# Kernel optimization log

Measured on AMD Instinct MI355X. Metric: run time of the kernel, lower is better.

The kernel has to match this reference:

```python
import jax, jax.numpy as jnp
import numpy as np

N_USERS = 30000
N_ITEMS = 20000
EMBED = 64
N_UI_LAYERS = 2
MASK_RATE = 0.1
MODEL_CAT = 0.02
USER_CAT = 0.3
ITEM_CAT = 0.3
NNZ = 600000


def setup_inputs() -> dict:
    key = jax.random.key(0)
    ks = jax.random.split(key, 16)
    ui_rows = jax.random.randint(ks[0], (NNZ,), 0, N_USERS, dtype=jnp.int64 if jax.config.jax_enable_x64 else jnp.int32)
    ui_cols = jax.random.randint(ks[1], (NNZ,), 0, N_ITEMS, dtype=ui_rows.dtype)
    ui_vals = jax.random.uniform(ks[2], (NNZ,), dtype=jnp.float32) * 0.1
    image_feats = jax.random.normal(ks[3], (N_ITEMS, 4096), dtype=jnp.float32)
    text_feats = jax.random.normal(ks[4], (N_ITEMS, 768), dtype=jnp.float32)
    user_feats0 = jax.random.normal(ks[5], (N_USERS, 1536), dtype=jnp.float32)
    item_title = jax.random.normal(ks[6], (N_ITEMS, 1536), dtype=jnp.float32)
    W_img = jax.random.normal(ks[7], (EMBED, 4096), dtype=jnp.float32) * 0.02
    b_img = jnp.zeros((EMBED,), jnp.float32)
    W_txt = jax.random.normal(ks[8], (EMBED, 768), dtype=jnp.float32) * 0.02
    b_txt = jnp.zeros((EMBED,), jnp.float32)
    W_usr = jax.random.normal(ks[9], (EMBED, 1536), dtype=jnp.float32) * 0.02
    b_usr = jnp.zeros((EMBED,), jnp.float32)
    W_itm = jax.random.normal(ks[10], (EMBED, 1536), dtype=jnp.float32) * 0.02
    b_itm = jnp.zeros((EMBED,), jnp.float32)
    user_id_emb = jax.random.normal(ks[11], (N_USERS, EMBED), dtype=jnp.float32) * 0.02
    item_id_emb = jax.random.normal(ks[12], (N_ITEMS, EMBED), dtype=jnp.float32) * 0.02
    return dict(ui_rows=ui_rows, ui_cols=ui_cols, ui_vals=ui_vals,
                image_feats=image_feats, text_feats=text_feats,
                user_feats0=user_feats0, item_title=item_title,
                W_img=W_img, b_img=b_img, W_txt=W_txt, b_txt=b_txt,
                W_usr=W_usr, b_usr=b_usr, W_itm=W_itm, b_itm=b_itm,
                user_id_emb=user_id_emb, item_id_emb=item_id_emb)


def _l2n(x):
    # F.normalize(x, p=2, dim=1)
    n = jnp.sqrt(jnp.sum(x * x, axis=1, keepdims=True))
    return x / jnp.maximum(n, 1e-12)


def reference(ui_rows, ui_cols, ui_vals, image_feats, text_feats, user_feats0, item_title,
              W_img, b_img, W_txt, b_txt, W_usr, b_usr, W_itm, b_itm,
              user_id_emb, item_id_emb):
    # sparse.mm(ui_graph, x): gather item rows, scale by edge vals, scatter-add to users
    def spmm_ui(x):
        return jax.ops.segment_sum(ui_vals[:, None] * x[ui_cols], ui_rows, num_segments=N_USERS)

    def spmm_iu(x):  # transpose graph
        return jax.ops.segment_sum(ui_vals[:, None] * x[ui_rows], ui_cols, num_segments=N_ITEMS)

    # --- feature masking (randperm with fixed key) ---
    num_mask = int(MASK_RATE * N_ITEMS)
    perm = jax.random.permutation(jax.random.key(42), N_ITEMS)
    mask_nodes = perm[:num_mask]
    img_m = image_feats.at[mask_nodes].set(image_feats.mean(0))
    txt_m = text_feats.at[mask_nodes].set(text_feats.mean(0))
    itm_m = item_title.at[mask_nodes].set(item_title.mean(0))

    # --- dense projections (dropout p=0 -> identity) ---
    raw_image = image_feats @ W_img.T + b_img
    raw_text = text_feats @ W_txt.T + b_txt
    raw_item = item_title @ W_itm.T + b_itm
    img_e = img_m @ W_img.T + b_img
    txt_e = txt_m @ W_txt.T + b_txt
    usr_e = user_feats0 @ W_usr.T + b_usr
    itm_e = itm_m @ W_itm.T + b_itm

    # --- modality graph propagation (args.layers=1; torch loop recomputes from fixed feats) ---
    image_user = spmm_ui(img_e)
    image_item = spmm_iu(image_user)
    text_user = spmm_ui(txt_e)
    text_item = spmm_iu(text_user)

    user_feat_from_item = spmm_ui(itm_e)
    item_feats_out = spmm_iu(user_feat_from_item)
    item_prof = spmm_iu(usr_e)
    user_prof = spmm_ui(item_prof)

    # --- id-embedding LightGCN-ish propagation ---
    u = user_id_emb
    i = item_id_emb
    u_list = [u]
    i_list = [i]
    for l in range(N_UI_LAYERS):
        if l == N_UI_LAYERS - 1:
            u = jax.nn.softmax(spmm_ui(i), axis=-1)
            i = jax.nn.softmax(spmm_iu(u), axis=-1)
        else:
            u = spmm_ui(i)
            i = spmm_iu(u)
        u_list.append(u)
        i_list.append(i)
    u_g = jnp.mean(jnp.stack(u_list), axis=0)
    i_g = jnp.mean(jnp.stack(i_list), axis=0)

    u_g = u_g + MODEL_CAT * _l2n(image_user) + MODEL_CAT * _l2n(text_user)
    i_g = i_g + MODEL_CAT * _l2n(image_item) + MODEL_CAT * _l2n(text_item)
    u_g = u_g + USER_CAT * _l2n(user_prof)
    i_g = i_g + USER_CAT * _l2n(item_prof)
    u_g = u_g + ITEM_CAT * _l2n(user_feat_from_item)
    i_g = i_g + ITEM_CAT * _l2n(item_feats_out)

    return (u_g, i_g, image_item, text_item, image_user, text_user, usr_e, item_feats_out,
            user_prof, item_prof, user_feat_from_item, mask_nodes,
            raw_image, raw_text, raw_item)
```

## Files before the change

kernel.cpp:

```cpp
#include <hip/hip_runtime.h>
#include <hip/hip_bf16.h>
#include <cstdint>
#include <cstddef>

#define NU 30000
#define NI 20000
#define NMASK 2000
#define NBUCK 2048

static inline int cdiv(int a, int b){ return (a + b - 1) / b; }

typedef __attribute__((ext_vector_type(8))) short bf16x8;
typedef __attribute__((ext_vector_type(4))) float f32x4;

__device__ __forceinline__ uint32_t rotl32(uint32_t x, int r){ return (x<<r)|(x>>(32-r)); }

__device__ __forceinline__ void tf2x32(uint32_t k0, uint32_t k1,
                                       uint32_t x0, uint32_t x1,
                                       uint32_t& o0, uint32_t& o1)
{
  uint32_t k2 = k0 ^ k1 ^ 0x1BD11BDAu;
  x0 += k0; x1 += k1;
#define TFR(r) { x0 += x1; x1 = rotl32(x1,(r)); x1 ^= x0; }
  TFR(13) TFR(15) TFR(26) TFR(6)
  x0 += k1; x1 += k2 + 1u;
  TFR(17) TFR(29) TFR(16) TFR(24)
  x0 += k2; x1 += k0 + 2u;
  TFR(13) TFR(15) TFR(26) TFR(6)
  x0 += k0; x1 += k1 + 3u;
  TFR(17) TFR(29) TFR(16) TFR(24)
  x0 += k1; x1 += k2 + 4u;
  TFR(13) TFR(15) TFR(26) TFR(6)
  x0 += k2; x1 += k0 + 5u;
#undef TFR
  o0 = x0; o1 = x1;
}

__device__ __forceinline__ ushort f2bf(float f){
  __hip_bfloat16 h = __float2bfloat16(f);
  return *reinterpret_cast<ushort*>(&h);
}
__device__ __forceinline__ uint32_t pk2(float a, float b){
  __hip_bfloat162 h = __float22bfloat162_rn(make_float2(a, b));
  return *reinterpret_cast<uint32_t*>(&h);
}
__device__ __forceinline__ uint2 f4_to_bf4(float4 v){
  __hip_bfloat162 h0 = __float22bfloat162_rn(make_float2(v.x, v.y));
  __hip_bfloat162 h1 = __float22bfloat162_rn(make_float2(v.z, v.w));
  return make_uint2(*reinterpret_cast<uint32_t*>(&h0), *reinterpret_cast<uint32_t*>(&h1));
}
__device__ __forceinline__ float lobf(uint32_t p){
  union { uint32_t u; float f; } c; c.u = p << 16; return c.f;
}
__device__ __forceinline__ float hibf(uint32_t p){
  union { uint32_t u; float f; } c; c.u = p & 0xffff0000u; return c.f;
}
__device__ __forceinline__ float bf2f(ushort h){
  union { uint32_t u; float f; } c; c.u = (uint32_t)h << 16; return c.f;
}

#define WTOTAL (64*(4096+768+1536+1536))
__global__ __launch_bounds__(256) void prep_kernel(
    uint32_t* __restrict__ bits1, uint32_t* __restrict__ bits2,
    int* __restrict__ h1, int* __restrict__ h2,
    const float* __restrict__ wi, const float* __restrict__ wt,
    const float* __restrict__ wm, const float* __restrict__ wu,
    ushort* __restrict__ wbf,
    const int* __restrict__ rows, const int* __restrict__ cols,
    int* __restrict__ cnt_u, int* __restrict__ cnt_i, int nnz)
{
  int i = blockIdx.x*256 + threadIdx.x;
  if (i < NI) {
    uint32_t c0,c1, s0,s1, t0,t1;
    tf2x32(0u,42u, 0u,0u, c0,c1);
    tf2x32(0u,42u, 0u,1u, s0,s1);
    tf2x32(c0,c1, 0u,1u, t0,t1);
    uint32_t o0,o1;
    tf2x32(s0,s1, 0u,(uint32_t)i, o0,o1);
    uint32_t b1 = o0^o1;
    tf2x32(t0,t1, 0u,(uint32_t)i, o0,o1);
    uint32_t b2 = o0^o1;
    bits1[i] = b1; bits2[i] = b2;
    atomicAdd(&h1[b1 >> 21], 1);
    atomicAdd(&h2[b2 >> 21], 1);
  }
  const int n0 = 64*4096, n1 = 64*768, n2 = 64*1536;
  for (int k = i; k < WTOTAL; k += gridDim.x*256) {
    float v;
    if (k < n0) v = wi[k];
    else if (k < n0+n1) v = wt[k-n0];
    else if (k < n0+n1+n2) v = wm[k-n0-n1];
    else v = wu[k-n0-n1-n2];
    wbf[k] = f2bf(v);
  }
  for (int k = i; k < nnz; k += gridDim.x*256) {
    atomicAdd(&cnt_u[rows[k]], 1);
    atomicAdd(&cnt_i[cols[k]], 1);
  }
}

__global__ __launch_bounds__(64) void exscan2_kernel(
    const int* __restrict__ h1, int* __restrict__ bb1,
    const int* __restrict__ h2, int* __restrict__ bb2)
{
  const int* cnt = blockIdx.x ? h2 : h1;
  int* ptr = blockIdx.x ? bb2 : bb1;
  int lane = threadIdx.x;
  int carry = 0;
  for (int base = 0; base < NBUCK; base += 64) {
    int i = base + lane;
    int v = cnt[i];
    int s = v;
#pragma unroll
    for (int off = 1; off < 64; off <<= 1) {
      int t = __shfl_up(s, off);
      if (lane >= off) s += t;
    }
    ptr[i] = carry + s - v;
    carry += __shfl(s, 63);
  }
  if (lane == 0) ptr[NBUCK] = carry;
}

__global__ __launch_bounds__(256) void scatter12_kernel(
    const uint32_t* __restrict__ bits1, const int* __restrict__ bb1, int* __restrict__ c1,
    uint64_t* __restrict__ barr1,
    const uint32_t* __restrict__ bits2, const int* __restrict__ bb2, int* __restrict__ c2,
    uint64_t* __restrict__ barr2, int n)
{
  int i = blockIdx.x*256 + threadIdx.x;
  if (i >= n) return;
  uint32_t k1 = bits1[i];
  int b = k1 >> 21;
  int p = bb1[b] + atomicAdd(&c1[b], 1);
  barr1[p] = ((uint64_t)k1 << 32) | (uint32_t)i;
  uint32_t k2 = bits2[i];
  b = k2 >> 21;
  p = bb2[b] + atomicAdd(&c2[b], 1);
  barr2[p] = ((uint64_t)k2 << 32) | (uint32_t)i;
}

template<int FINAL>
__global__ __launch_bounds__(256) void rank_bucket_kernel(
    const uint64_t* __restrict__ barr, const int* __restrict__ bptr,
    uint32_t* __restrict__ perm, float* __restrict__ mask_out, int* __restrict__ flag,
    int n)
{
  int p = blockIdx.x*256 + threadIdx.x;
  if (p >= n) return;
  uint64_t mk = barr[p];
  int b = (int)(mk >> 53);
  int p0 = bptr[b], p1 = bptr[b+1];
  int r = p0;
  for (int q = p0; q < p1; ++q) r += (int)(barr[q] < mk);
  uint32_t i = (uint32_t)mk;
  if (!FINAL) {
    perm[r] = i;
  } else if (r < NMASK) {
    uint32_t v = perm[i];
    mask_out[r] = (float)v;
    flag[v] = 1;
  }
}

#define RB_I 313
#define RB_U 469
__global__ __launch_bounds__(256) void gemm_all_kernel(
    const float* __restrict__ Xi, const float* __restrict__ Xt,
    const float* __restrict__ Xm, const float* __restrict__ Xu,
    const ushort* __restrict__ wbf,
    ushort* __restrict__ pb_img, ushort* __restrict__ pb_txt,
    ushort* __restrict__ pb_itm, ushort* __restrict__ pb_usr)
{
  __shared__ ushort Xs[64][72];
  __shared__ ushort Ws[64][72];
  const int bid = blockIdx.x;
  const float* X; const ushort* Wbf; ushort* pb;
  int N, K, klen, rb, ch;
  if (bid < RB_I*8) {
    X = Xi; Wbf = wbf; pb = pb_img; N = NI; K = 4096; klen = 512;
    rb = bid % RB_I; ch = bid / RB_I;
  } else if (bid < RB_I*12) {
    int l = bid - RB_I*8;
    X = Xt; Wbf = wbf + 64*4096; pb = pb_txt; N = NI; K = 768; klen = 192;
    rb = l % RB_I; ch = l / RB_I;
  } else if (bid < RB_I*16) {
    int l = bid - RB_I*12;
    X = Xm; Wbf = wbf + 64*(4096+768); pb = pb_itm; N = NI; K = 1536; klen = 384;
    rb = l % RB_I; ch = l / RB_I;
  } else {
    int l = bid - RB_I*16;
    X = Xu; Wbf = wbf + 64*(4096+768+1536); pb = pb_usr; N = NU; K = 1536; klen = 256;
    rb = l % RB_U; ch = l / RB_U;
  }
  const int tid = threadIdx.x;
  const int row0 = rb * 64;
  const int kbeg = ch * klen;
  const int lane = tid & 63;
  const int wr = tid >> 6;
  const int lrow = lane & 15;
  const int kslot = lane >> 4;
  f32x4 acc[4] = {f32x4{0,0,0,0},f32x4{0,0,0,0},f32x4{0,0,0,0},f32x4{0,0,0,0}};

  const int sr = tid >> 4;
  const int sc = (tid & 15) * 4;
  const int wrow = tid >> 2;
  const int wcol = (tid & 3) * 16;

  for (int k0 = kbeg; k0 < kbeg + klen; k0 += 64) {
#pragma unroll
    for (int i = 0; i < 4; ++i) {
      int r = sr + 16*i;
      int gr = row0 + r;
      float4 v = make_float4(0.f,0.f,0.f,0.f);
      if (gr < N) v = *reinterpret_cast<const float4*>(X + (size_t)gr*K + k0 + sc);
      *reinterpret_cast<uint2*>(&Xs[r][sc]) = f4_to_bf4(v);
    }
    {
      const ushort* wsrc = Wbf + (size_t)wrow*K + k0 + wcol;
      *reinterpret_cast<uint4*>(&Ws[wrow][wcol])   = *reinterpret_cast<const uint4*>(wsrc);
      *reinterpret_cast<uint4*>(&Ws[wrow][wcol+8]) = *reinterpret_cast<const uint4*>(wsrc + 8);
    }
    __syncthreads();
#pragma unroll
    for (int ks = 0; ks < 2; ++ks) {
      int kb = ks*32 + kslot*8;
      bf16x8 af = *reinterpret_cast<const bf16x8*>(&Xs[wr*16 + lrow][kb]);
#pragma unroll
      for (int ct = 0; ct < 4; ++ct) {
        bf16x8 bfr = *reinterpret_cast<const bf16x8*>(&Ws[ct*16 + lrow][kb]);
        acc[ct] = __builtin_amdgcn_mfma_f32_16x16x32_bf16(af, bfr, acc[ct], 0, 0, 0);
      }
    }
    __syncthreads();
  }
  ushort* pbc = pb + (size_t)ch * N * 64;
#pragma unroll
  for (int ct = 0; ct < 4; ++ct)
#pragma unroll
    for (int j = 0; j < 4; ++j) {
      int gr = row0 + wr*16 + kslot*4 + j;
      if (gr < N) pbc[(size_t)gr*64 + ct*16 + lrow] = f2bf(acc[ct][j]);
    }
}

__global__ __launch_bounds__(256) void reduce4_kernel(
    const ushort* __restrict__ pb_img, const ushort* __restrict__ pb_txt,
    const ushort* __restrict__ pb_itm, const ushort* __restrict__ pb_usr,
    const float* __restrict__ b_img, const float* __restrict__ b_txt,
    const float* __restrict__ b_itm, const float* __restrict__ b_usr,
    const float* __restrict__ idemb,
    float* __restrict__ o_ri, float* __restrict__ o_rt, float* __restrict__ o_rit,
    float* __restrict__ o_ue, ushort* __restrict__ ue_bf,
    uint2* __restrict__ pk_all, float* __restrict__ means)
{
  __shared__ float red[3][256];
  const int nI = NI*64, nUx = NU*64;
  int lane = threadIdx.x & 63;
  float sa = 0.f, sb = 0.f, sc = 0.f;
  for (int i = blockIdx.x*256 + threadIdx.x; i < nUx; i += gridDim.x*256) {
    int lc = i & 63;
    if (i < nI) {
      float s = b_img[lc];
#pragma unroll
      for (int c = 0; c < 8; ++c) s += bf2f(pb_img[(size_t)c*nI + i]);
      o_ri[i] = s;
      float t = b_txt[lc];
#pragma unroll
      for (int c = 0; c < 4; ++c) t += bf2f(pb_txt[(size_t)c*nI + i]);
      o_rt[i] = t;
      float u = b_itm[lc];
#pragma unroll
      for (int c = 0; c < 4; ++c) u += bf2f(pb_itm[(size_t)c*nI + i]);
      o_rit[i] = u;
      pk_all[i] = make_uint2(pk2(s, t), pk2(u, idemb[i]));
      sa += s; sb += t; sc += u;
    }
    float su = b_usr[lc];
#pragma unroll
    for (int c = 0; c < 6; ++c) su += bf2f(pb_usr[(size_t)c*nUx + i]);
    o_ue[i] = su; ue_bf[i] = f2bf(su);
  }
  red[0][threadIdx.x] = sa; red[1][threadIdx.x] = sb; red[2][threadIdx.x] = sc;
  __syncthreads();
  if (threadIdx.x < 64) {
#pragma unroll
    for (int q = 0; q < 3; ++q) {
      float t = red[q][lane]+red[q][64+lane]+red[q][128+lane]+red[q][192+lane];
      if (t != 0.f) atomicAdd(&means[q*64+lane], t * (1.f/NI));
    }
  }
}

__global__ __launch_bounds__(256) void scan_block2_kernel(
    const int* __restrict__ cnt_u, const int* __restrict__ cnt_i,
    int* __restrict__ part_u, int* __restrict__ part_i,
    int* __restrict__ bsum_u, int* __restrict__ bsum_i, int nbu)
{
  __shared__ int wsum[4];
  bool isU = (int)blockIdx.x < nbu;
  int blk = isU ? blockIdx.x : blockIdx.x - nbu;
  const int* cnt = isU ? cnt_u : cnt_i;
  int* part = isU ? part_u : part_i;
  int* bsum = isU ? bsum_u : bsum_i;
  int n = isU ? NU : NI;
  int i = blk*256 + threadIdx.x;
  int lane = threadIdx.x & 63;
  int w = threadIdx.x >> 6;
  int v = (i < n) ? cnt[i] : 0;
  int s = v;
#pragma unroll
  for (int off = 1; off < 64; off <<= 1) {
    int t = __shfl_up(s, off);
    if (lane >= off) s += t;
  }
  if (lane == 63) wsum[w] = s;
  __syncthreads();
  int wo = 0;
#pragma unroll
  for (int k = 0; k < 4; ++k) if (k < w) wo += wsum[k];
  if (i < n) part[i] = wo + s - v;
  if (threadIdx.x == 255) bsum[blk] = wo + s;
}

__global__ __launch_bounds__(64) void exscan2b_kernel(
    const int* __restrict__ bs_u, int* __restrict__ bp_u, int nbu,
    const int* __restrict__ bs_i, int* __restrict__ bp_i, int nbi)
{
  const int* cnt = blockIdx.x ? bs_i : bs_u;
  int* ptr = blockIdx.x ? bp_i : bp_u;
  int n = blockIdx.x ? nbi : nbu;
  int lane = threadIdx.x;
  int carry = 0;
  for (int base = 0; base < n; base += 64) {
    int i = base + lane;
    int v = (i < n) ? cnt[i] : 0;
    int s = v;
#pragma unroll
    for (int off = 1; off < 64; off <<= 1) {
      int t = __shfl_up(s, off);
      if (lane >= off) s += t;
    }
    if (i < n) ptr[i] = carry + s - v;
    carry += __shfl(s, 63);
  }
  if (lane == 0) ptr[n] = carry;
}

__global__ __launch_bounds__(256) void scan_add2_kernel(
    const int* __restrict__ part_u, const int* __restrict__ bp_u,
    const int* __restrict__ part_i, const int* __restrict__ bp_i,
    int* __restrict__ ptr_u, int* __restrict__ cur_u,
    int* __restrict__ ptr_i, int* __restrict__ cur_i, int nbu, int nbi)
{
  bool isU = (int)blockIdx.x < nbu;
  int blk = isU ? blockIdx.x : blockIdx.x - nbu;
  int n = isU ? NU : NI;
  const int* part = isU ? part_u : part_i;
  const int* bp = isU ? bp_u : bp_i;
  int* ptr = isU ? ptr_u : ptr_i;
  int* cur = isU ? cur_u : cur_i;
  int i = blk*256 + threadIdx.x;
  if (i < n) { int v = part[i] + bp[blk]; ptr[i] = v; cur[i] = v; }
  if (i == 0) ptr[n] = bp[isU ? nbu : nbi];
}

__global__ __launch_bounds__(256) void scatter_kernel(
    const int* __restrict__ rows, const int* __restrict__ cols, const float* __restrict__ vals,
    int* __restrict__ cur_u, int* __restrict__ cur_i,
    int* __restrict__ idx_u, float* __restrict__ val_u,
    int* __restrict__ idx_i, float* __restrict__ val_i, int nnz)
{
  int k = blockIdx.x*256 + threadIdx.x;
  if (k < nnz) {
    int r = rows[k], c = cols[k];
    float v = vals[k];
    int pu = atomicAdd(&cur_u[r], 1);
    idx_u[pu] = c; val_u[pu] = v;
    int pi = atomicAdd(&cur_i[c], 1);
    idx_i[pi] = r; val_i[pi] = v;
  }
}

__global__ __launch_bounds__(256) void spmm_user1_kernel(
    const int* __restrict__ ptr, const int* __restrict__ idx, const float* __restrict__ val,
    const uint2* __restrict__ pka,
    const int* __restrict__ flag, const float* __restrict__ means,
    float* __restrict__ iu, float* __restrict__ tu, float* __restrict__ ufi, float* __restrict__ u1,
    uint2* __restrict__ qa, int nrows)
{
  int row = blockIdx.x*4 + (threadIdx.x >> 6);
  int lane = threadIdx.x & 63;
  if (row >= nrows) return;
  int p0 = ptr[row], p1 = ptr[row+1];
  float m0 = means[lane], m1 = means[64+lane], m2 = means[128+lane];
  float a0=0.f, a1=0.f, a2=0.f, a3=0.f;
#define U1STEP(gg,ff,ww) { float x0,x1,x2, x3 = hibf(gg.y); \
    if (ff) { x0=m0; x1=m1; x2=m2; } \
    else { x0=lobf(gg.x); x1=hibf(gg.x); x2=lobf(gg.y); } \
    a0=fmaf(ww,x0,a0); a1=fmaf(ww,x1,a1); a2=fmaf(ww,x2,a2); a3=fmaf(ww,x3,a3); }
  int p = p0;
  for (; p + 8 <= p1; p += 8) {
    int j[8]; float w[8]; int f[8]; uint2 g[8];
#pragma unroll
    for (int q = 0; q < 8; ++q) { j[q]=idx[p+q]; w[q]=val[p+q]; }
#pragma unroll
    for (int q = 0; q < 8; ++q) { f[q]=flag[j[q]]; g[q]=pka[(size_t)j[q]*64+lane]; }
#pragma unroll
    for (int q = 0; q < 8; ++q) U1STEP(g[q],f[q],w[q])
  }
  for (; p + 4 <= p1; p += 4) {
    int j0=idx[p+0], j1=idx[p+1], j2=idx[p+2], j3=idx[p+3];
    float w0=val[p+0], w1=val[p+1], w2=val[p+2], w3=val[p+3];
    int f0=flag[j0], f1=flag[j1], f2=flag[j2], f3=flag[j3];
    uint2 g0=pka[(size_t)j0*64+lane], g1=pka[(size_t)j1*64+lane];
    uint2 g2=pka[(size_t)j2*64+lane], g3=pka[(size_t)j3*64+lane];
    U1STEP(g0,f0,w0) U1STEP(g1,f1,w1) U1STEP(g2,f2,w2) U1STEP(g3,f3,w3)
  }
  for (; p < p1; ++p) {
    int j = idx[p]; float v = val[p];
    uint2 g = pka[(size_t)j*64 + lane];
    int f = flag[j];
    U1STEP(g,f,v)
  }
#undef U1STEP
  size_t o = (size_t)row*64 + lane;
  iu[o]=a0; tu[o]=a1; ufi[o]=a2; u1[o]=a3;
  qa[o] = make_uint2(pk2(a0, a1), pk2(a2, a3));
}

__global__ __launch_bounds__(256) void spmm_item1_kernel(
    const int* __restrict__ ptr, const int* __restrict__ idx, const float* __restrict__ val,
    const uint2* __restrict__ qa, const ushort* __restrict__ ueh,
    float* __restrict__ ii, float* __restrict__ ti, float* __restrict__ ifo,
    float* __restrict__ i1, float* __restrict__ ip,
    uint32_t* __restrict__ qip1, int nrows)
{
  int row = blockIdx.x*4 + (threadIdx.x >> 6);
  int lane = threadIdx.x & 63;
  if (row >= nrows) return;
  int p0 = ptr[row], p1 = ptr[row+1];
  float a0=0.f, a1=0.f, a2=0.f, a3=0.f, a4=0.f;
#define I1STEP(gg,uu,ww) { \
    a0=fmaf(ww,lobf(gg.x),a0); a1=fmaf(ww,hibf(gg.x),a1); \
    a2=fmaf(ww,lobf(gg.y),a2); a3=fmaf(ww,hibf(gg.y),a3); \
    a4=fmaf(ww,bf2f(uu),a4); }
  int p = p0;
  for (; p + 8 <= p1; p += 8) {
    int j[8]; float w[8]; uint2 g[8]; ushort u[8];
#pragma unroll
    for (int q = 0; q < 8; ++q) { j[q]=idx[p+q]; w[q]=val[p+q]; }
#pragma unroll
    for (int q = 0; q < 8; ++q) {
      size_t b = (size_t)j[q]*64+lane;
      g[q]=qa[b]; u[q]=ueh[b];
    }
#pragma unroll
    for (int q = 0; q < 8; ++q) I1STEP(g[q],u[q],w[q])
  }
  for (; p + 4 <= p1; p += 4) {
    int j0=idx[p+0], j1=idx[p+1], j2=idx[p+2], j3=idx[p+3];
    float w0=val[p+0], w1=val[p+1], w2=val[p+2], w3=val[p+3];
    size_t b0=(size_t)j0*64+lane, b1=(size_t)j1*64+lane, b2=(size_t)j2*64+lane, b3=(size_t)j3*64+lane;
    uint2 g0=qa[b0], g1=qa[b1], g2=qa[b2], g3=qa[b3];
    ushort u0=ueh[b0], u1_=ueh[b1], u2_=ueh[b2], u3_=ueh[b3];
    I1STEP(g0,u0,w0) I1STEP(g1,u1_,w1) I1STEP(g2,u2_,w2) I1STEP(g3,u3_,w3)
  }
  for (; p < p1; ++p) {
    int j = idx[p]; float v = val[p];
    size_t b = (size_t)j*64 + lane;
    uint2 g = qa[b]; ushort u = ueh[b];
    I1STEP(g,u,v)
  }
#undef I1STEP
  size_t o = (size_t)row*64 + lane;
  ii[o]=a0; ti[o]=a1; ifo[o]=a2; i1[o]=a3; ip[o]=a4;
  qip1[o] = pk2(a4, a3);
}

__global__ __launch_bounds__(256) void user2_kernel(
    const int* __restrict__ ptr, const int* __restrict__ idx, const float* __restrict__ val,
    const uint32_t* __restrict__ qip1,
    const float* __restrict__ idemb, const float* __restrict__ u1,
    const float* __restrict__ iu, const float* __restrict__ tu, const float* __restrict__ ufi,
    float* __restrict__ up, ushort* __restrict__ u2h, float* __restrict__ ug, int nrows)
{
  int row = blockIdx.x*4 + (threadIdx.x >> 6);
  int lane = threadIdx.x & 63;
  if (row >= nrows) return;
  int p0 = ptr[row], p1 = ptr[row+1];
  float aup=0.f, au2=0.f;
  int p = p0;
  for (; p + 4 <= p1; p += 4) {
    int j0=idx[p+0], j1=idx[p+1], j2=idx[p+2], j3=idx[p+3];
    float w0=val[p+0], w1=val[p+1], w2=val[p+2], w3=val[p+3];
    uint32_t g0=qip1[(size_t)j0*64+lane], g1=qip1[(size_t)j1*64+lane];
    uint32_t g2=qip1[(size_t)j2*64+lane], g3=qip1[(size_t)j3*64+lane];
    aup=fmaf(w0,lobf(g0),aup); au2=fmaf(w0,hibf(g0),au2);
    aup=fmaf(w1,lobf(g1),aup); au2=fmaf(w1,hibf(g1),au2);
    aup=fmaf(w2,lobf(g2),aup); au2=fmaf(w2,hibf(g2),au2);
    aup=fmaf(w3,lobf(g3),aup); au2=fmaf(w3,hibf(g3),au2);
  }
  for (; p < p1; ++p) {
    int j = idx[p]; float v = val[p];
    uint32_t g = qip1[(size_t)j*64 + lane];
    aup = fmaf(v, lobf(g), aup);
    au2 = fmaf(v, hibf(g), au2);
  }
  float m = au2;
#pragma unroll
  for (int o2=32;o2;o2>>=1) m = fmaxf(m, __shfl_xor(m, o2));
  float e = expf(au2 - m);
  float s = e;
#pragma unroll
  for (int o2=32;o2;o2>>=1) s += __shfl_xor(s, o2);
  float u2 = e / s;
  size_t o = (size_t)row*64 + lane;
  up[o] = aup; u2h[o] = f2bf(u2);
  float e0 = idemb[o], e1 = u1[o];
  float v1 = iu[o], v2 = tu[o], v3 = aup, v4 = ufi[o];
  float n1=v1*v1, n2=v2*v2, n3=v3*v3, n4=v4*v4;
#pragma unroll
  for (int o2=32;o2;o2>>=1) {
    n1 += __shfl_xor(n1, o2); n2 += __shfl_xor(n2, o2);
    n3 += __shfl_xor(n3, o2); n4 += __shfl_xor(n4, o2);
  }
  n1 = fmaxf(sqrtf(n1), 1e-12f); n2 = fmaxf(sqrtf(n2), 1e-12f);
  n3 = fmaxf(sqrtf(n3), 1e-12f); n4 = fmaxf(sqrtf(n4), 1e-12f);
  ug[o] = (e0+e1+u2)*(1.f/3.f)
        + 0.02f*(v1/n1) + 0.02f*(v2/n2)
        + 0.30f*(v3/n3) + 0.30f*(v4/n4);
}

__global__ __launch_bounds__(256) void item2_kernel(
    const int* __restrict__ ptr, const int* __restrict__ idx, const float* __restrict__ val,
    const ushort* __restrict__ u2h,
    const float* __restrict__ idemb, const float* __restrict__ i1,
    const float* __restrict__ ii, const float* __restrict__ ti,
    const float* __restrict__ ip, const float* __restrict__ ifo,
    float* __restrict__ ig, int nrows)
{
  int row = blockIdx.x*4 + (threadIdx.x >> 6);
  int lane = threadIdx.x & 63;
  if (row >= nrows) return;
  int p0 = ptr[row], p1 = ptr[row+1];
  float ai2=0.f;
  int p = p0;
  for (; p + 4 <= p1; p += 4) {
    int j0=idx[p+0], j1=idx[p+1], j2=idx[p+2], j3=idx[p+3];
    float w0=val[p+0], w1=val[p+1], w2=val[p+2], w3=val[p+3];
    ushort h0=u2h[(size_t)j0*64+lane], h1=u2h[(size_t)j1*64+lane];
    ushort h2=u2h[(size_t)j2*64+lane], h3=u2h[(size_t)j3*64+lane];
    ai2=fmaf(w0,bf2f(h0),ai2); ai2=fmaf(w1,bf2f(h1),ai2);
    ai2=fmaf(w2,bf2f(h2),ai2); ai2=fmaf(w3,bf2f(h3),ai2);
  }
  for (; p < p1; ++p) {
    int j = idx[p]; float v = val[p];
    ai2 = fmaf(v, bf2f(u2h[(size_t)j*64 + lane]), ai2);
  }
  float m = ai2;
#pragma unroll
  for (int o2=32;o2;o2>>=1) m = fmaxf(m, __shfl_xor(m, o2));
  float e = expf(ai2 - m);
  float s = e;
#pragma unroll
  for (int o2=32;o2;o2>>=1) s += __shfl_xor(s, o2);
  float i2 = e / s;
  size_t o = (size_t)row*64 + lane;
  float e0 = idemb[o], e1 = i1[o];
  float v1 = ii[o], v2 = ti[o], v3 = ip[o], v4 = ifo[o];
  float n1=v1*v1, n2=v2*v2, n3=v3*v3, n4=v4*v4;
#pragma unroll
  for (int o2=32;o2;o2>>=1) {
    n1 += __shfl_xor(n1, o2); n2 += __shfl_xor(n2, o2);
    n3 += __shfl_xor(n3, o2); n4 += __shfl_xor(n4, o2);
  }
  n1 = fmaxf(sqrtf(n1), 1e-12f); n2 = fmaxf(sqrtf(n2), 1e-12f);
  n3 = fmaxf(sqrtf(n3), 1e-12f); n4 = fmaxf(sqrtf(n4), 1e-12f);
  ig[o] = (e0+e1+i2)*(1.f/3.f)
        + 0.02f*(v1/n1) + 0.02f*(v2/n2)
        + 0.30f*(v3/n3) + 0.30f*(v4/n4);
}

extern "C" void kernel_launch(void* const* d_in, const int* in_sizes, int n_in,
                              void* d_out, int out_size, void* d_ws, size_t ws_size,
                              hipStream_t stream)
{
  const int*   ui_rows     = (const int*)d_in[0];
  const int*   ui_cols     = (const int*)d_in[1];
  const float* ui_vals     = (const float*)d_in[2];
  const float* image_feats = (const float*)d_in[3];
  const float* text_feats  = (const float*)d_in[4];
  const float* user_feats0 = (const float*)d_in[5];
  const float* item_title  = (const float*)d_in[6];
  const float* W_img = (const float*)d_in[7];
  const float* b_img = (const float*)d_in[8];
  const float* W_txt = (const float*)d_in[9];
  const float* b_txt = (const float*)d_in[10];
  const float* W_usr = (const float*)d_in[11];
  const float* b_usr = (const float*)d_in[12];
  const float* W_itm = (const float*)d_in[13];
  const float* b_itm = (const float*)d_in[14];
  const float* user_id_emb = (const float*)d_in[15];
  const float* item_id_emb = (const float*)d_in[16];
  const int nnz = in_sizes[0];

  float* out = (float*)d_out;
  const size_t OU = (size_t)NU*64, OI = (size_t)NI*64;
  size_t off = 0;
  float* o_ug   = out + off; off += OU;
  float* o_ig   = out + off; off += OI;
  float* o_ii   = out + off; off += OI;
  float* o_ti   = out + off; off += OI;
  float* o_iu   = out + off; off += OU;
  float* o_tu   = out + off; off += OU;
  float* o_ue   = out + off; off += OU;
  float* o_ifo  = out + off; off += OI;
  float* o_up   = out + off; off += OU;
  float* o_ip   = out + off; off += OI;
  float* o_ufi  = out + off; off += OU;
  float* o_mask = out + off; off += NMASK;
  float* o_ri   = out + off; off += OI;
  float* o_rt   = out + off; off += OI;
  float* o_rit  = out + off; off += OI;

  char* wp = (char*)d_ws;
  auto walloc = [&](size_t bytes) -> char* {
    char* r = wp; wp += (bytes + 255) & ~(size_t)255; return r;
  };
  int*   cnt_u = (int*)  walloc((size_t)NU*4);
  int*   cnt_i = (int*)  walloc((size_t)NI*4);
  int*   flag  = (int*)  walloc((size_t)NI*4);
  float* means = (float*)walloc(3*64*4);
  int*   h1    = (int*)  walloc(NBUCK*4);
  int*   c1    = (int*)  walloc(NBUCK*4);
  int*   h2    = (int*)  walloc(NBUCK*4);
  int*   c2    = (int*)  walloc(NBUCK*4);
  size_t zero_bytes = (size_t)(wp - (char*)d_ws);
  uint32_t* bits1 = (uint32_t*)walloc((size_t)NI*4);
  uint32_t* bits2 = (uint32_t*)walloc((size_t)NI*4);
  uint32_t* permA = (uint32_t*)walloc((size_t)NI*4);
  uint64_t* barr1 = (uint64_t*)walloc((size_t)NI*8);
  uint64_t* barr2 = (uint64_t*)walloc((size_t)NI*8);
  int*   bb1   = (int*)  walloc((NBUCK+1)*4);
  int*   bb2   = (int*)  walloc((NBUCK+1)*4);
  int*   ptr_u = (int*)  walloc((size_t)(NU+1)*4);
  int*   ptr_i = (int*)  walloc((size_t)(NI+1)*4);
  int*   cur_u = (int*)  walloc((size_t)NU*4);
  int*   cur_i = (int*)  walloc((size_t)NI*4);
  int*   idx_u = (int*)  walloc((size_t)nnz*4);
  float* val_u = (float*)walloc((size_t)nnz*4);
  int*   idx_i = (int*)  walloc((size_t)nnz*4);
  float* val_i = (float*)walloc((size_t)nnz*4);
  float* u1    = (float*)walloc(OU*4);
  float* i1    = (float*)walloc(OI*4);
  int*   part_u = (int*) walloc((size_t)NU*4);
  int*   part_i = (int*) walloc((size_t)NI*4);
  int*   bsum_u = (int*) walloc(128*4);
  int*   bsum_i = (int*) walloc(128*4);
  int*   bp_u   = (int*) walloc(129*4);
  int*   bp_i   = (int*) walloc(129*4);
  ushort* wbf  = (ushort*)walloc((size_t)WTOTAL*2);
  uint2* pk_all = (uint2*)walloc(OI*8);
  uint2* q_all  = (uint2*)walloc(OU*8);
  uint32_t* qip1 = (uint32_t*)walloc(OI*4);
  ushort*   ue_bf = (ushort*)walloc(OU*2);
  ushort*   u2h   = (ushort*)walloc(OU*2);
  ushort* pb_img = (ushort*)walloc((size_t)8*NI*64*2);
  ushort* pb_txt = (ushort*)walloc((size_t)4*NI*64*2);
  ushort* pb_itm = (ushort*)walloc((size_t)4*NI*64*2);
  ushort* pb_usr = (ushort*)walloc((size_t)6*NU*64*2);

  hipMemsetAsync(d_ws, 0, zero_bytes, stream);

  prep_kernel<<<512, 256, 0, stream>>>(bits1, bits2, h1, h2,
      W_img, W_txt, W_itm, W_usr, wbf, ui_rows, ui_cols, cnt_u, cnt_i, nnz);

  const int GB = cdiv(NI,256);
  exscan2_kernel<<<2, 64, 0, stream>>>(h1, bb1, h2, bb2);
  scatter12_kernel<<<GB, 256, 0, stream>>>(bits1, bb1, c1, barr1, bits2, bb2, c2, barr2, NI);
  rank_bucket_kernel<0><<<GB, 256, 0, stream>>>(barr1, bb1, permA, nullptr, nullptr, NI);
  rank_bucket_kernel<1><<<GB, 256, 0, stream>>>(barr2, bb2, permA, o_mask, flag, NI);

  gemm_all_kernel<<<RB_I*16 + RB_U*6, 256, 0, stream>>>(
      image_feats, text_feats, item_title, user_feats0, wbf,
      pb_img, pb_txt, pb_itm, pb_usr);
  reduce4_kernel<<<1024, 256, 0, stream>>>(pb_img, pb_txt, pb_itm, pb_usr,
      b_img, b_txt, b_itm, b_usr, item_id_emb,
      o_ri, o_rt, o_rit, o_ue, ue_bf, pk_all, means);

  {
    int nbu = cdiv(NU,256), nbi = cdiv(NI,256);
    scan_block2_kernel<<<nbu+nbi, 256, 0, stream>>>(cnt_u, cnt_i, part_u, part_i, bsum_u, bsum_i, nbu);
    exscan2b_kernel<<<2, 64, 0, stream>>>(bsum_u, bp_u, nbu, bsum_i, bp_i, nbi);
    scan_add2_kernel<<<nbu+nbi, 256, 0, stream>>>(part_u, bp_u, part_i, bp_i,
        ptr_u, cur_u, ptr_i, cur_i, nbu, nbi);
  }
  scatter_kernel<<<cdiv(nnz,256), 256, 0, stream>>>(ui_rows, ui_cols, ui_vals,
      cur_u, cur_i, idx_u, val_u, idx_i, val_i, nnz);

  const int GU = cdiv(NU,4), GI = cdiv(NI,4);
  spmm_user1_kernel<<<GU,256,0,stream>>>(ptr_u, idx_u, val_u,
      pk_all, flag, means,
      o_iu, o_tu, o_ufi, u1, q_all, NU);
  spmm_item1_kernel<<<GI,256,0,stream>>>(ptr_i, idx_i, val_i,
      q_all, ue_bf,
      o_ii, o_ti, o_ifo, i1, o_ip, qip1, NI);
  user2_kernel<<<GU,256,0,stream>>>(ptr_u, idx_u, val_u,
      qip1, user_id_emb, u1, o_iu, o_tu, o_ufi,
      o_up, u2h, o_ug, NU);
  item2_kernel<<<GI,256,0,stream>>>(ptr_i, idx_i, val_i,
      u2h, item_id_emb, i1, o_ii, o_ti, o_ip, o_ifo,
      o_ig, NI);
}
```

Measured before the change: 540.1 us.

## Load GEMM activations straight into MFMA registers, stage whole W chunk once

The fused projection GEMM no longer stages X through shared memory. Each lane now loads its own fp32 row slice directly from global memory, converts it to bf16 and feeds the MFMA. The weight slice for the whole 256-wide K chunk is loaded into LDS once, which removes the per-iteration barriers. K chunks are made uniform at 256, which raises the split-K count for image and item-title features and changes the partial buffers and reduction counts to match. This cuts LDS traffic and synchronisation, but global loads are now less coalesced (strided per lane), and the reduction has to read more partial data.

```diff
diff --git a/kernel.cpp b/kernel.cpp
--- a/kernel.cpp
+++ b/kernel.cpp
@@ -49,6 +49,11 @@
   __hip_bfloat162 h1 = __float22bfloat162_rn(make_float2(v.z, v.w));
   return make_uint2(*reinterpret_cast<uint32_t*>(&h0), *reinterpret_cast<uint32_t*>(&h1));
 }
+__device__ __forceinline__ bf16x8 f8_to_bf8(float4 a, float4 b){
+  uint2 c = f4_to_bf4(a), d = f4_to_bf4(b);
+  uint4 u = make_uint4(c.x, c.y, d.x, d.y);
+  return *reinterpret_cast<bf16x8*>(&u);
+}
 __device__ __forceinline__ float lobf(uint32_t p){
   union { uint32_t u; float f; } c; c.u = p << 16; return c.f;
 }
@@ -163,8 +168,11 @@
   }
 }
 
-#define RB_I 313
-#define RB_U 469
+#define KLEN 256
+#define SEG0 (313*16)
+#define SEG1 (SEG0 + 313*3)
+#define SEG2 (SEG1 + 313*6)
+#define SEG3 (SEG2 + 469*6)
 __global__ __launch_bounds__(256) void gemm_all_kernel(
     const float* __restrict__ Xi, const float* __restrict__ Xt,
     const float* __restrict__ Xm, const float* __restrict__ Xu,
@@ -172,67 +180,69 @@
     ushort* __restrict__ pb_img, ushort* __restrict__ pb_txt,
     ushort* __restrict__ pb_itm, ushort* __restrict__ pb_usr)
 {
-  __shared__ ushort Xs[64][72];
-  __shared__ ushort Ws[64][72];
+  __shared__ ushort Ws[64][KLEN + 8];
   const int bid = blockIdx.x;
   const float* X; const ushort* Wbf; ushort* pb;
-  int N, K, klen, rb, ch;
-  if (bid < RB_I*8) {
-    X = Xi; Wbf = wbf; pb = pb_img; N = NI; K = 4096; klen = 512;
-    rb = bid % RB_I; ch = bid / RB_I;
-  } else if (bid < RB_I*12) {
-    int l = bid - RB_I*8;
-    X = Xt; Wbf = wbf + 64*4096; pb = pb_txt; N = NI; K = 768; klen = 192;
-    rb = l % RB_I; ch = l / RB_I;
-  } else if (bid < RB_I*16) {
-    int l = bid - RB_I*12;
-    X = Xm; Wbf = wbf + 64*(4096+768); pb = pb_itm; N = NI; K = 1536; klen = 384;
-    rb = l % RB_I; ch = l / RB_I;
+  int N, K, rb, ch;
+  if (bid < SEG0) {
+    X = Xi; Wbf = wbf; pb = pb_img; N = NI; K = 4096;
+    rb = bid % 313; ch = bid / 313;
+  } else if (bid < SEG1) {
+    int l = bid - SEG0;
+    X = Xt; Wbf = wbf + 64*4096; pb = pb_txt; N = NI; K = 768;
+    rb = l % 313; ch = l / 313;
+  } else if (bid < SEG2) {
+    int l = bid - SEG1;
+    X = Xm; Wbf = wbf + 64*(4096+768); pb = pb_itm; N = NI; K = 1536;
+    rb = l % 313; ch = l / 313;
   } else {
-    int l = bid - RB_I*16;
-    X = Xu; Wbf = wbf + 64*(4096+768+1536); pb = pb_usr; N = NU; K = 1536; klen = 256;
-    rb = l % RB_U; ch = l / RB_U;
+    int l = bid - SEG2;
+    X = Xu; Wbf = wbf + 64*(4096+768+1536); pb = pb_usr; N = NU; K = 1536;
+    rb = l % 469; ch = l / 469;
   }
   const int tid = threadIdx.x;
   const int row0 = rb * 64;
-  const int kbeg = ch * klen;
+  const int kbeg = ch * KLEN;
   const int lane = tid & 63;
   const int wr = tid >> 6;
   const int lrow = lane & 15;
   const int kslot = lane >> 4;
+
+  {
+    const int wrow = tid >> 2;
+    const int wcol = (tid & 3) * 64;
+    const ushort* wsrc = Wbf + (size_t)wrow*K + kbeg + wcol;
+#pragma unroll
+    for (int i = 0; i < 8; ++i)
+      *reinterpret_cast<uint4*>(&Ws[wrow][wcol + i*8]) =
+        *reinterpret_cast<const uint4*>(wsrc + i*8);
+  }
+  __syncthreads();
+
   f32x4 acc[4] = {f32x4{0,0,0,0},f32x4{0,0,0,0},f32x4{0,0,0,0},f32x4{0,0,0,0}};
-
-  const int sr = tid >> 4;
-  const int sc = (tid & 15) * 4;
-  const int wrow = tid >> 2;
-  const int wcol = (tid & 3) * 16;
-
-  for (int k0 = kbeg; k0 < kbeg + klen; k0 += 64) {
-#pragma unroll
-    for (int i = 0; i < 4; ++i) {
-      int r = sr + 16*i;
-      int gr = row0 + r;
-      float4 v = make_float4(0.f,0.f,0.f,0.f);
-      if (gr < N) v = *reinterpret_cast<const float4*>(X + (size_t)gr*K + k0 + sc);
-      *reinterpret_cast<uint2*>(&Xs[r][sc]) = f4_to_bf4(v);
+  const int myrow = row0 + wr*16 + lrow;
+  const bool live = (myrow < N);
+  const float* xrow = X + (size_t)(live ? myrow : 0)*K + kbeg + kslot*8;
+
+#pragma unroll
+  for (int k0 = 0; k0 < KLEN; k0 += 64) {
+    float4 z = make_float4(0.f,0.f,0.f,0.f);
+    float4 xa0 = z, xa1 = z, xb0 = z, xb1 = z;
+    if (live) {
+      xa0 = *reinterpret_cast<const float4*>(xrow + k0);
+      xa1 = *reinterpret_cast<const float4*>(xrow + k0 + 4);
+      xb0 = *reinterpret_cast<const float4*>(xrow + k0 + 32);
+      xb1 = *reinterpret_cast<const float4*>(xrow + k0 + 36);
     }
-    {
-      const ushort* wsrc = Wbf + (size_t)wrow*K + k0 + wcol;
-      *reinterpret_cast<uint4*>(&Ws[wrow][wcol])   = *reinterpret_cast<const uint4*>(wsrc);
-      *reinterpret_cast<uint4*>(&Ws[wrow][wcol+8]) = *reinterpret_cast<const uint4*>(wsrc + 8);
+    bf16x8 a0 = f8_to_bf8(xa0, xa1);
+    bf16x8 a1 = f8_to_bf8(xb0, xb1);
+#pragma unroll
+    for (int ct = 0; ct < 4; ++ct) {
+      bf16x8 b0 = *reinterpret_cast<const bf16x8*>(&Ws[ct*16 + lrow][k0 + kslot*8]);
+      bf16x8 b1 = *reinterpret_cast<const bf16x8*>(&Ws[ct*16 + lrow][k0 + 32 + kslot*8]);
+      acc[ct] = __builtin_amdgcn_mfma_f32_16x16x32_bf16(a0, b0, acc[ct], 0, 0, 0);
+      acc[ct] = __builtin_amdgcn_mfma_f32_16x16x32_bf16(a1, b1, acc[ct], 0, 0, 0);
     }
-    __syncthreads();
-#pragma unroll
-    for (int ks = 0; ks < 2; ++ks) {
-      int kb = ks*32 + kslot*8;
-      bf16x8 af = *reinterpret_cast<const bf16x8*>(&Xs[wr*16 + lrow][kb]);
-#pragma unroll
-      for (int ct = 0; ct < 4; ++ct) {
-        bf16x8 bfr = *reinterpret_cast<const bf16x8*>(&Ws[ct*16 + lrow][kb]);
-        acc[ct] = __builtin_amdgcn_mfma_f32_16x16x32_bf16(af, bfr, acc[ct], 0, 0, 0);
-      }
-    }
-    __syncthreads();
   }
   ushort* pbc = pb + (size_t)ch * N * 64;
 #pragma unroll
@@ -263,15 +273,15 @@
     if (i < nI) {
       float s = b_img[lc];
 #pragma unroll
-      for (int c = 0; c < 8; ++c) s += bf2f(pb_img[(size_t)c*nI + i]);
+      for (int c = 0; c < 16; ++c) s += bf2f(pb_img[(size_t)c*nI + i]);
       o_ri[i] = s;
       float t = b_txt[lc];
 #pragma unroll
-      for (int c = 0; c < 4; ++c) t += bf2f(pb_txt[(size_t)c*nI + i]);
+      for (int c = 0; c < 3; ++c) t += bf2f(pb_txt[(size_t)c*nI + i]);
       o_rt[i] = t;
       float u = b_itm[lc];
 #pragma unroll
-      for (int c = 0; c < 4; ++c) u += bf2f(pb_itm[(size_t)c*nI + i]);
+      for (int c = 0; c < 6; ++c) u += bf2f(pb_itm[(size_t)c*nI + i]);
       o_rit[i] = u;
       pk_all[i] = make_uint2(pk2(s, t), pk2(u, idemb[i]));
       sa += s; sb += t; sc += u;
@@ -666,9 +676,9 @@
   uint32_t* qip1 = (uint32_t*)walloc(OI*4);
   ushort*   ue_bf = (ushort*)walloc(OU*2);
   ushort*   u2h   = (ushort*)walloc(OU*2);
-  ushort* pb_img = (ushort*)walloc((size_t)8*NI*64*2);
-  ushort* pb_txt = (ushort*)walloc((size_t)4*NI*64*2);
-  ushort* pb_itm = (ushort*)walloc((size_t)4*NI*64*2);
+  ushort* pb_img = (ushort*)walloc((size_t)16*NI*64*2);
+  ushort* pb_txt = (ushort*)walloc((size_t)3*NI*64*2);
+  ushort* pb_itm = (ushort*)walloc((size_t)6*NI*64*2);
   ushort* pb_usr = (ushort*)walloc((size_t)6*NU*64*2);
 
   hipMemsetAsync(d_ws, 0, zero_bytes, stream);
@@ -682,7 +692,7 @@
   rank_bucket_kernel<0><<<GB, 256, 0, stream>>>(barr1, bb1, permA, nullptr, nullptr, NI);
   rank_bucket_kernel<1><<<GB, 256, 0, stream>>>(barr2, bb2, permA, o_mask, flag, NI);
 
-  gemm_all_kernel<<<RB_I*16 + RB_U*6, 256, 0, stream>>>(
+  gemm_all_kernel<<<SEG3, 256, 0, stream>>>(
       image_feats, text_feats, item_title, user_feats0, wbf,
       pb_img, pb_txt, pb_itm, pb_usr);
   reduce4_kernel<<<1024, 256, 0, stream>>>(pb_img, pb_txt, pb_itm, pb_usr,
```

Result: no change. 546.1 us (+1.1%).
